# Kernel optimization log

Hardware: AMD Instinct MI355X
Metric: run time of the kernel (lower is better)

Reference implementation:

```python
import jax, jax.numpy as jnp
import numpy as np

B, T, F, N = 256, 1024, 16, 1024  # batch, history len, features, output_steps (num_nodes)


def setup_inputs() -> dict:
    key = jax.random.key(0)
    ks = jax.random.split(key, 12)
    he = lambda k, shape, fan_in: jax.random.normal(k, shape, jnp.float32) * np.sqrt(2.0 / fan_in)
    return {
        "history_in": jax.random.normal(ks[0], (B, T, F), jnp.float32),
        "node_id_in": jax.random.randint(ks[1], (B,), 0, N),
        "time_of_day_in": jax.random.randint(ks[2], (B,), 0, 288),
        "day_in_week_in": jax.random.randint(ks[3], (B,), 0, 7),
        "wt1": jax.random.uniform(ks[4], (1,), jnp.float32),
        "wt2": jax.random.uniform(ks[5], (1,), jnp.float32),
        "wt3": jax.random.uniform(ks[6], (1,), jnp.float32),
        "wt4": jax.random.uniform(ks[7], (1,), jnp.float32),
        # stacked per-feature Dense params: [F, T, N] weights, [F, N] biases
        "trend_W": he(ks[8], (F, T, N), T),
        "trend_b": jnp.zeros((F, N), jnp.float32),
        "residual_W": he(ks[9], (F, T, N), T),
        "residual_b": jnp.zeros((F, N), jnp.float32),
    }


def reference(history_in, node_id_in, time_of_day_in, day_in_week_in,
              wt1, wt2, wt3, wt4, trend_W, trend_b, residual_W, residual_b):
    x = history_in  # [B, T, F]
    # TF AveragePooling1D(pool_size=2, strides=1, padding='same'):
    # out[t] = mean(x[t], x[t+1]) for t < T-1; out[T-1] = x[T-1] (padding excluded from count)
    trend = jnp.concatenate([(x[:, :-1] + x[:, 1:]) * 0.5, x[:, -1:]], axis=1)  # [B, T, F]
    residual = x - trend
    # per-feature Dense (T -> N) for trend and residual, fused as batched GEMM over F
    out = (jnp.einsum('btf,ftn->bnf', trend, trend_W) + trend_b.T[None]
           + jnp.einsum('btf,ftn->bnf', residual, residual_W) + residual_b.T[None])  # [B, N, F]
    return out
```

## Files before the change

### kernel.cpp

```cpp
#include <hip/hip_runtime.h>
#include <hip/hip_bf16.h>
#include <stdint.h>

#define B_  256
#define T_  1024
#define F_  16
#define N_  1024

typedef short bf16x8 __attribute__((ext_vector_type(8)));
typedef float f32x4  __attribute__((ext_vector_type(4)));

static __device__ __forceinline__ unsigned short f2bf(float x) {
  unsigned u = __builtin_bit_cast(unsigned, x);
  u += 0x7fffu + ((u >> 16) & 1u);
  return (unsigned short)(u >> 16);
}
static __device__ __forceinline__ float bf2f(unsigned short h) {
  unsigned u = ((unsigned)h) << 16;
  return __builtin_bit_cast(float, u);
}

__global__ __launch_bounds__(256) void prep2_kernel(const float* __restrict__ x,
                                                    unsigned short* __restrict__ At2) {
  __shared__ unsigned short ld[16 * 1028];
  const int rb = blockIdx.x >> 4, tc = blockIdx.x & 15;
  const int tid = threadIdx.x;
  const int tl = tid >> 2;
  const int f4 = (tid & 3) * 4;
#pragma unroll
  for (int i = 0; i < 16; ++i) {
    const float* src = x + (((size_t)(rb * 16 + i) * T_) + tc * 64 + tl) * F_ + f4;
    float4 v = *(const float4*)src;
    uint2 pk;
    pk.x = (unsigned)f2bf(v.x) | ((unsigned)f2bf(v.y) << 16);
    pk.y = (unsigned)f2bf(v.z) | ((unsigned)f2bf(v.w) << 16);
    *(uint2*)&ld[i * 1028 + tl * 16 + f4] = pk;
  }
  __syncthreads();
  const int w = tid >> 6, l = tid & 63;
#pragma unroll
  for (int it = 0; it < 8; ++it) {
    const int c = it * 4 + w;
    const int f = c >> 1, kcl = c & 1;
    unsigned short t16[8];
#pragma unroll
    for (int j = 0; j < 8; ++j)
      t16[j] = ld[(l & 15) * 1028 + (kcl * 32 + ((l >> 4) * 8) + j) * 16 + f];
    uint4 q;
    q.x = (unsigned)t16[0] | ((unsigned)t16[1] << 16);
    q.y = (unsigned)t16[2] | ((unsigned)t16[3] << 16);
    q.z = (unsigned)t16[4] | ((unsigned)t16[5] << 16);
    q.w = (unsigned)t16[6] | ((unsigned)t16[7] << 16);
    *(uint4*)(At2 + (((size_t)(f * 32 + tc * 2 + kcl) * 16 + rb) << 9) + l * 8) = q;
  }
}

template <int TMPOUT>
__global__ __launch_bounds__(1024) void gemm_kernel(const unsigned short* __restrict__ At2,
                                                    const float* __restrict__ TW,
                                                    const float* __restrict__ RW,
                                                    const float* __restrict__ tb,
                                                    const float* __restrict__ rb,
                                                    float* __restrict__ out,
                                                    unsigned short* __restrict__ tmp) {
  __shared__ float rawT[64 * 64];
  __shared__ float rawR[64 * 64];
  __shared__ unsigned short vT[64 * 72];
  __shared__ float prevT[2][64], prevR[2][64];

  const int tid = threadIdx.x;
  const int bid = (blockIdx.x & 7) * 32 + (blockIdx.x >> 3);
  const int f  = bid >> 4;
  const int n0 = (bid & 15) * 64;
  const int w = tid >> 6, l = tid & 63;
  const int lrow = l & 15, lg = l >> 4;

  const float* TWf = TW + (size_t)f * (T_ * N_) + n0;
  const float* RWf = RW + (size_t)f * (T_ * N_) + n0;
  const unsigned short* Af2 = At2 + ((size_t)f * 32 * 16 * 512);

  const int wrow = tid >> 4;
  const int wc   = (tid & 15) * 4;

  f32x4 acc[4];
#pragma unroll
  for (int nt = 0; nt < 4; ++nt)
    acc[nt] = (f32x4){0.f, 0.f, 0.f, 0.f};

  float4 wtT = *(const float4*)(TWf + (size_t)wrow * N_ + wc);
  float4 wtR = *(const float4*)(RWf + (size_t)wrow * N_ + wc);
  bf16x8 afrag[2][2];
#pragma unroll
  for (int ks = 0; ks < 2; ++ks)
    afrag[0][ks] = *(const bf16x8*)(Af2 + (((size_t)(ks * 16 + w)) << 9) + l * 8);

#pragma unroll
  for (int kt = 0; kt < 16; ++kt) {
    const int k0 = kt * 64;
    __syncthreads();
    *(float4*)&rawT[wrow * 64 + wc] = wtT;
    *(float4*)&rawR[wrow * 64 + wc] = wtR;
    __syncthreads();
    if (kt < 15) {
      wtT = *(const float4*)(TWf + (size_t)(k0 + 64 + wrow) * N_ + wc);
      wtR = *(const float4*)(RWf + (size_t)(k0 + 64 + wrow) * N_ + wc);
#pragma unroll
      for (int ks = 0; ks < 2; ++ks)
        afrag[(kt + 1) & 1][ks] =
            *(const bf16x8*)(Af2 + (((size_t)(((kt + 1) * 2 + ks) * 16 + w)) << 9) + l * 8);
    }
    {
      float ptw, prw;
      if (w == 0) { ptw = prevT[(kt & 1) ^ 1][l]; prw = prevR[(kt & 1) ^ 1][l]; }
      else        { ptw = rawT[(w * 4 - 1) * 64 + l]; prw = rawR[(w * 4 - 1) * 64 + l]; }
      unsigned pk[2];
      unsigned lo32 = 0;
      float tw = 0.f, rw = 0.f;
#pragma unroll
      for (int i = 0; i < 4; ++i) {
        const int t = w * 4 + i, tg = k0 + t;
        tw = rawT[t * 64 + l]; rw = rawR[t * 64 + l];
        const float c1 = (tg < T_ - 1) ? 0.5f : 1.0f;
        const float c2 = (tg < T_ - 1) ? 0.5f : 0.0f;
        const float pterm = (tg >= 1) ? 0.5f * (ptw - prw) : 0.0f;
        const unsigned short us = f2bf(c1 * tw + c2 * rw + pterm);
        if ((i & 1) == 0) lo32 = us; else pk[i >> 1] = lo32 | ((unsigned)us << 16);
        ptw = tw; prw = rw;
      }
      uint2 q; q.x = pk[0]; q.y = pk[1];
      *(uint2*)&vT[l * 72 + w * 4] = q;
      if (w == 15) { prevT[kt & 1][l] = tw; prevR[kt & 1][l] = rw; }
    }
    __syncthreads();
#pragma unroll
    for (int ks = 0; ks < 2; ++ks) {
#pragma unroll
      for (int nt = 0; nt < 4; ++nt) {
        bf16x8 bfrag = *(const bf16x8*)&vT[(nt * 16 + lrow) * 72 + ks * 32 + lg * 8];
        acc[nt] = __builtin_amdgcn_mfma_f32_16x16x32_bf16(afrag[kt & 1][ks], bfrag, acc[nt], 0, 0, 0);
      }
    }
  }

#pragma unroll
  for (int nt = 0; nt < 4; ++nt) {
    const int n = n0 + nt * 16 + lrow;
    const float bsum = tb[f * N_ + n] + rb[f * N_ + n];
#pragma unroll
    for (int j = 0; j < 4; ++j) {
      const int brow = w * 16 + lg * 4 + j;
      const float v = acc[nt][j] + bsum;
      if (TMPOUT) {
        tmp[((size_t)f * B_ + brow) * N_ + n] = f2bf(v);
      } else {
        out[((size_t)brow * N_ + n) * F_ + f] = v;
      }
    }
  }
}

__global__ __launch_bounds__(256) void untile_kernel(const unsigned short* __restrict__ tmp,
                                                     float* __restrict__ out) {
  __shared__ unsigned short ld[16 * 1048];
  const int b = blockIdx.x, tid = threadIdx.x;
#pragma unroll
  for (int it = 0; it < 8; ++it) {
    const int idx = it * 256 + tid;
    const int f = idx >> 7, c = idx & 127;
    uint4 v = *(const uint4*)(tmp + ((size_t)f * B_ + b) * N_ + c * 8);
    *(uint4*)&ld[f * 1048 + c * 8] = v;
  }
  __syncthreads();
  float* ob = out + (size_t)b * (N_ * F_);
#pragma unroll
  for (int it = 0; it < 16; ++it) {
    const int g = it * 256 + tid;
    const int n = g >> 2, f0 = (g & 3) * 4;
    float4 o;
    o.x = bf2f(ld[(f0 + 0) * 1048 + n]);
    o.y = bf2f(ld[(f0 + 1) * 1048 + n]);
    o.z = bf2f(ld[(f0 + 2) * 1048 + n]);
    o.w = bf2f(ld[(f0 + 3) * 1048 + n]);
    *(float4*)(ob + n * F_ + f0) = o;
  }
}

extern "C" void kernel_launch(void* const* d_in, const int* in_sizes, int n_in,
                              void* d_out, int out_size, void* d_ws, size_t ws_size,
                              hipStream_t stream) {
  const float* x  = (const float*)d_in[0];
  const float* TW = (const float*)d_in[8];
  const float* tb = (const float*)d_in[9];
  const float* RW = (const float*)d_in[10];
  const float* rb = (const float*)d_in[11];
  float* out = (float*)d_out;

  unsigned short* At2 = (unsigned short*)d_ws;
  const size_t atBytes  = (size_t)F_ * B_ * T_ * sizeof(unsigned short);
  const size_t tmpBytes = (size_t)F_ * B_ * N_ * sizeof(unsigned short);

  prep2_kernel<<<256, 256, 0, stream>>>(x, At2);
  if (ws_size >= atBytes + tmpBytes) {
    unsigned short* tmp = (unsigned short*)((char*)d_ws + atBytes);
    gemm_kernel<1><<<256, 1024, 0, stream>>>(At2, TW, RW, tb, rb, out, tmp);
    untile_kernel<<<256, 256, 0, stream>>>(tmp, out);
  } else {
    gemm_kernel<0><<<256, 1024, 0, stream>>>(At2, TW, RW, tb, rb, out, nullptr);
  }
}
```

Baseline: 41.89 us.

## Restructure GEMM into two large K-phases with direct weight loads and fragment-ordered LDS

Replaces the 16-step K loop, which staged raw fp32 weights through LDS with per-step barriers, with two phases of 512 K each. In each phase every wave loads its 32 weight rows straight from global memory and builds the combined bf16 B operand in registers. It writes that operand into LDS in MFMA fragment order, so the B fragment reads become contiguous. This cuts barriers and LDS traffic, at the cost of removing register prefetch overlap between loads and MFMAs and using scalar strided LDS stores.

After: 44.28 us. 1.06x slower.

```diff
diff --git a/kernel.cpp b/kernel.cpp
--- a/kernel.cpp
+++ b/kernel.cpp
@@ -63,10 +63,7 @@
                                                     const float* __restrict__ rb,
                                                     float* __restrict__ out,
                                                     unsigned short* __restrict__ tmp) {
-  __shared__ float rawT[64 * 64];
-  __shared__ float rawR[64 * 64];
-  __shared__ unsigned short vT[64 * 72];
-  __shared__ float prevT[2][64], prevR[2][64];
+  __shared__ unsigned short vT[16 * 4 * 64 * 8];
 
   const int tid = threadIdx.x;
   const int bid = (blockIdx.x & 7) * 32 + (blockIdx.x >> 3);
@@ -79,65 +76,49 @@
   const float* RWf = RW + (size_t)f * (T_ * N_) + n0;
   const unsigned short* Af2 = At2 + ((size_t)f * 32 * 16 * 512);
 
-  const int wrow = tid >> 4;
-  const int wc   = (tid & 15) * 4;
-
   f32x4 acc[4];
 #pragma unroll
   for (int nt = 0; nt < 4; ++nt)
     acc[nt] = (f32x4){0.f, 0.f, 0.f, 0.f};
 
-  float4 wtT = *(const float4*)(TWf + (size_t)wrow * N_ + wc);
-  float4 wtR = *(const float4*)(RWf + (size_t)wrow * N_ + wc);
-  bf16x8 afrag[2][2];
 #pragma unroll
-  for (int ks = 0; ks < 2; ++ks)
-    afrag[0][ks] = *(const bf16x8*)(Af2 + (((size_t)(ks * 16 + w)) << 9) + l * 8);
-
+  for (int p = 0; p < 2; ++p) {
+    const int t0 = p * 512 + w * 32;
+    float ptw = 0.f, prw = 0.f;
+    if (t0 > 0) {
+      ptw = TWf[(size_t)(t0 - 1) * N_ + l];
+      prw = RWf[(size_t)(t0 - 1) * N_ + l];
+    }
+    __syncthreads();
 #pragma unroll
-  for (int kt = 0; kt < 16; ++kt) {
-    const int k0 = kt * 64;
-    __syncthreads();
-    *(float4*)&rawT[wrow * 64 + wc] = wtT;
-    *(float4*)&rawR[wrow * 64 + wc] = wtR;
-    __syncthreads();
-    if (kt < 15) {
-      wtT = *(const float4*)(TWf + (size_t)(k0 + 64 + wrow) * N_ + wc);
-      wtR = *(const float4*)(RWf + (size_t)(k0 + 64 + wrow) * N_ + wc);
+    for (int b = 0; b < 4; ++b) {
+      float tw8[8], rw8[8];
 #pragma unroll
-      for (int ks = 0; ks < 2; ++ks)
-        afrag[(kt + 1) & 1][ks] =
-            *(const bf16x8*)(Af2 + (((size_t)(((kt + 1) * 2 + ks) * 16 + w)) << 9) + l * 8);
-    }
-    {
-      float ptw, prw;
-      if (w == 0) { ptw = prevT[(kt & 1) ^ 1][l]; prw = prevR[(kt & 1) ^ 1][l]; }
-      else        { ptw = rawT[(w * 4 - 1) * 64 + l]; prw = rawR[(w * 4 - 1) * 64 + l]; }
-      unsigned pk[2];
-      unsigned lo32 = 0;
-      float tw = 0.f, rw = 0.f;
+      for (int i = 0; i < 8; ++i) {
+        tw8[i] = TWf[(size_t)(t0 + b * 8 + i) * N_ + l];
+        rw8[i] = RWf[(size_t)(t0 + b * 8 + i) * N_ + l];
+      }
 #pragma unroll
-      for (int i = 0; i < 4; ++i) {
-        const int t = w * 4 + i, tg = k0 + t;
-        tw = rawT[t * 64 + l]; rw = rawR[t * 64 + l];
+      for (int i = 0; i < 8; ++i) {
+        const int tl = b * 8 + i;
+        const int tg = t0 + tl;
         const float c1 = (tg < T_ - 1) ? 0.5f : 1.0f;
         const float c2 = (tg < T_ - 1) ? 0.5f : 0.0f;
         const float pterm = (tg >= 1) ? 0.5f * (ptw - prw) : 0.0f;
-        const unsigned short us = f2bf(c1 * tw + c2 * rw + pterm);
-        if ((i & 1) == 0) lo32 = us; else pk[i >> 1] = lo32 | ((unsigned)us << 16);
-        ptw = tw; prw = rw;
+        vT[((w * 4 + (l >> 4)) * 64 + (tl >> 3) * 16 + (l & 15)) * 8 + (tl & 7)] =
+            f2bf(c1 * tw8[i] + c2 * rw8[i] + pterm);
+        ptw = tw8[i]; prw = rw8[i];
       }
-      uint2 q; q.x = pk[0]; q.y = pk[1];
-      *(uint2*)&vT[l * 72 + w * 4] = q;
-      if (w == 15) { prevT[kt & 1][l] = tw; prevR[kt & 1][l] = rw; }
     }
     __syncthreads();
 #pragma unroll
-    for (int ks = 0; ks < 2; ++ks) {
+    for (int kcl = 0; kcl < 16; ++kcl) {
+      const int kc = p * 16 + kcl;
+      bf16x8 a = *(const bf16x8*)(Af2 + (((size_t)(kc * 16 + w)) << 9) + l * 8);
 #pragma unroll
       for (int nt = 0; nt < 4; ++nt) {
-        bf16x8 bfrag = *(const bf16x8*)&vT[(nt * 16 + lrow) * 72 + ks * 32 + lg * 8];
-        acc[nt] = __builtin_amdgcn_mfma_f32_16x16x32_bf16(afrag[kt & 1][ks], bfrag, acc[nt], 0, 0, 0);
+        bf16x8 bfrag = *(const bf16x8*)&vT[((kcl * 4 + nt) * 64 + l) * 8];
+        acc[nt] = __builtin_amdgcn_mfma_f32_16x16x32_bf16(a, bfrag, acc[nt], 0, 0, 0);
       }
     }
   }
```

## Stream weight tiles directly into double-buffered LDS and drop a barrier per step

Applied to the files above, without the earlier changes.

Weight tiles now go straight from global memory into LDS through global_load_lds instead of being staged through registers. The raw-weight and vT LDS buffers are double-buffered, so the next tile's load overlaps the current tile's preprocessing and MFMA work. This removes the per-iteration register-to-LDS store and one of the two __syncthreads per k-step. In exchange LDS use roughly doubles, the kernel relies on correct vmcnt waits before the barrier, and launch_bounds(1024,4) adds a register-pressure hint that may limit allocation.

Result: slower. 44.43 us (+6.1%).

```diff
diff --git a/kernel.cpp b/kernel.cpp
--- a/kernel.cpp
+++ b/kernel.cpp
@@ -18,6 +18,10 @@
 static __device__ __forceinline__ float bf2f(unsigned short h) {
   unsigned u = ((unsigned)h) << 16;
   return __builtin_bit_cast(float, u);
+}
+static __device__ __forceinline__ void gload16(const void* g, void* l) {
+  __builtin_amdgcn_global_load_lds((const __attribute__((address_space(1))) void*)g,
+                                   (__attribute__((address_space(3))) void*)l, 16, 0, 0);
 }
 
 __global__ __launch_bounds__(256) void prep2_kernel(const float* __restrict__ x,
@@ -56,16 +60,16 @@
 }
 
 template <int TMPOUT>
-__global__ __launch_bounds__(1024) void gemm_kernel(const unsigned short* __restrict__ At2,
-                                                    const float* __restrict__ TW,
-                                                    const float* __restrict__ RW,
-                                                    const float* __restrict__ tb,
-                                                    const float* __restrict__ rb,
-                                                    float* __restrict__ out,
-                                                    unsigned short* __restrict__ tmp) {
-  __shared__ float rawT[64 * 64];
-  __shared__ float rawR[64 * 64];
-  __shared__ unsigned short vT[64 * 72];
+__global__ __launch_bounds__(1024, 4) void gemm_kernel(const unsigned short* __restrict__ At2,
+                                                       const float* __restrict__ TW,
+                                                       const float* __restrict__ RW,
+                                                       const float* __restrict__ tb,
+                                                       const float* __restrict__ rb,
+                                                       float* __restrict__ out,
+                                                       unsigned short* __restrict__ tmp) {
+  __shared__ float rawT[2][64 * 64];
+  __shared__ float rawR[2][64 * 64];
+  __shared__ unsigned short vT[2][64 * 72];
   __shared__ float prevT[2][64], prevR[2][64];
 
   const int tid = threadIdx.x;
@@ -79,47 +83,44 @@
   const float* RWf = RW + (size_t)f * (T_ * N_) + n0;
   const unsigned short* Af2 = At2 + ((size_t)f * 32 * 16 * 512);
 
-  const int wrow = tid >> 4;
-  const int wc   = (tid & 15) * 4;
+  const size_t gsrc = (size_t)(w * 4 + (l >> 4)) * N_ + (l & 15) * 4;
 
   f32x4 acc[4];
 #pragma unroll
   for (int nt = 0; nt < 4; ++nt)
     acc[nt] = (f32x4){0.f, 0.f, 0.f, 0.f};
 
-  float4 wtT = *(const float4*)(TWf + (size_t)wrow * N_ + wc);
-  float4 wtR = *(const float4*)(RWf + (size_t)wrow * N_ + wc);
+  gload16(TWf + gsrc, &rawT[0][w * 256]);
+  gload16(RWf + gsrc, &rawR[0][w * 256]);
   bf16x8 afrag[2][2];
 #pragma unroll
   for (int ks = 0; ks < 2; ++ks)
     afrag[0][ks] = *(const bf16x8*)(Af2 + (((size_t)(ks * 16 + w)) << 9) + l * 8);
+  __syncthreads();
 
 #pragma unroll
   for (int kt = 0; kt < 16; ++kt) {
     const int k0 = kt * 64;
-    __syncthreads();
-    *(float4*)&rawT[wrow * 64 + wc] = wtT;
-    *(float4*)&rawR[wrow * 64 + wc] = wtR;
-    __syncthreads();
+    const int cur = kt & 1, nxt = cur ^ 1;
     if (kt < 15) {
-      wtT = *(const float4*)(TWf + (size_t)(k0 + 64 + wrow) * N_ + wc);
-      wtR = *(const float4*)(RWf + (size_t)(k0 + 64 + wrow) * N_ + wc);
+      gload16(TWf + (size_t)(k0 + 64) * N_ + gsrc, &rawT[nxt][w * 256]);
+      gload16(RWf + (size_t)(k0 + 64) * N_ + gsrc, &rawR[nxt][w * 256]);
 #pragma unroll
       for (int ks = 0; ks < 2; ++ks)
-        afrag[(kt + 1) & 1][ks] =
+        afrag[nxt][ks] =
             *(const bf16x8*)(Af2 + (((size_t)(((kt + 1) * 2 + ks) * 16 + w)) << 9) + l * 8);
     }
     {
       float ptw, prw;
-      if (w == 0) { ptw = prevT[(kt & 1) ^ 1][l]; prw = prevR[(kt & 1) ^ 1][l]; }
-      else        { ptw = rawT[(w * 4 - 1) * 64 + l]; prw = rawR[(w * 4 - 1) * 64 + l]; }
+      if (w == 0) { ptw = prevT[cur ^ 1][l]; prw = prevR[cur ^ 1][l]; }
+      else        { ptw = rawT[cur][(w * 4 - 1) * 64 + l]; prw = rawR[cur][(w * 4 - 1) * 64 + l]; }
       unsigned pk[2];
       unsigned lo32 = 0;
       float tw = 0.f, rw = 0.f;
 #pragma unroll
       for (int i = 0; i < 4; ++i) {
         const int t = w * 4 + i, tg = k0 + t;
-        tw = rawT[t * 64 + l]; rw = rawR[t * 64 + l];
+        tw = rawT[cur][t * 64 + l]; rw = rawR[cur][t * 64 + l];
         const float c1 = (tg < T_ - 1) ? 0.5f : 1.0f;
         const float c2 = (tg < T_ - 1) ? 0.5f : 0.0f;
         const float pterm = (tg >= 1) ? 0.5f * (ptw - prw) : 0.0f;
@@ -128,16 +129,16 @@
         ptw = tw; prw = rw;
       }
       uint2 q; q.x = pk[0]; q.y = pk[1];
-      *(uint2*)&vT[l * 72 + w * 4] = q;
-      if (w == 15) { prevT[kt & 1][l] = tw; prevR[kt & 1][l] = rw; }
+      *(uint2*)&vT[cur][l * 72 + w * 4] = q;
+      if (w == 15) { prevT[cur][l] = tw; prevR[cur][l] = rw; }
     }
     __syncthreads();
 #pragma unroll
     for (int ks = 0; ks < 2; ++ks) {
 #pragma unroll
       for (int nt = 0; nt < 4; ++nt) {
-        bf16x8 bfrag = *(const bf16x8*)&vT[(nt * 16 + lrow) * 72 + ks * 32 + lg * 8];
-        acc[nt] = __builtin_amdgcn_mfma_f32_16x16x32_bf16(afrag[kt & 1][ks], bfrag, acc[nt], 0, 0, 0);
+        bf16x8 bfrag = *(const bf16x8*)&vT[cur][(nt * 16 + lrow) * 72 + ks * 32 + lg * 8];
+        acc[nt] = __builtin_amdgcn_mfma_f32_16x16x32_bf16(afrag[cur][ks], bfrag, acc[nt], 0, 0, 0);
       }
     }
   }
```
